# Kernel tuning notes

Measured on AMD Instinct MI355X. Metric: run time of the kernel, lower is better.

## Reference

```python
import jax, jax.numpy as jnp
import numpy as np

N_NODES = 50000
N_EDGES = 800000
NFEAT = 128
NHID = 64  # gc1: NFEAT -> 2*NHID, gc2: 2*NHID -> NHID


def setup_inputs() -> dict:
    key = jax.random.key(0)
    k1, k2, k3, k4, k5 = jax.random.split(key, 5)
    feat = jax.random.normal(k1, (N_NODES, NFEAT), dtype=jnp.float32)
    src = jax.random.randint(k2, (N_EDGES,), 0, N_NODES, dtype=jnp.int32)
    dst = jax.random.randint(k3, (N_EDGES,), 0, N_NODES, dtype=jnp.int32)
    # GraphConv weights: (in_feats, out_feats), xavier-like scale
    W1 = jax.random.normal(k4, (NFEAT, 2 * NHID), dtype=jnp.float32) / np.sqrt(NFEAT)
    b1 = jnp.zeros((2 * NHID,), dtype=jnp.float32)
    W2 = jax.random.normal(k5, (2 * NHID, NHID), dtype=jnp.float32) / np.sqrt(2 * NHID)
    b2 = jnp.zeros((NHID,), dtype=jnp.float32)
    return {"feat": feat, "src": src, "dst": dst, "W1": W1, "b1": b1, "W2": W2, "b2": b2}


def _graph_conv(feat, src, dst, W, b):
    """DGL GraphConv, norm='both', allow_zero_in_degree=True.
    h = D_in^{-1/2} A (D_out^{-1/2} x) W + b, with degrees clamped to >= 1.
    Applies W before aggregation when in_feats > out_feats (saves bandwidth)."""
    N = feat.shape[0]
    ones = jnp.ones(src.shape[0], dtype=feat.dtype)
    deg_out = jnp.clip(jax.ops.segment_sum(ones, src, num_segments=N), 1.0)
    deg_in = jnp.clip(jax.ops.segment_sum(ones, dst, num_segments=N), 1.0)
    h = feat * (deg_out ** -0.5)[:, None]
    mult_first = W.shape[0] > W.shape[1]
    if mult_first:
        h = h @ W
    agg = jax.ops.segment_sum(h[src], dst, num_segments=N)  # [N, d]
    if not mult_first:
        agg = agg @ W
    return agg * (deg_in ** -0.5)[:, None] + b


def reference(feat, src, dst, W1, b1, W2, b2):
    x = jax.nn.relu(_graph_conv(feat, src, dst, W1, b1))
    # dropout is inactive in eval mode (F.dropout training=False)
    x = _graph_conv(x, src, dst, W2, b2)
    return jax.nn.log_softmax(x, axis=1)
```

## Files before the change

### kernel.cpp

```cpp
#include <hip/hip_runtime.h>
#include <math.h>


constexpr int NF   = 128;
constexpr int NH   = 64;
constexpr int CAP  = 48;
constexpr int EPB  = 4096;
constexpr int BCAP = 8192;
constexpr int NBKMAX = 256;

typedef unsigned int uint;
typedef unsigned short ushort_t;
typedef __attribute__((ext_vector_type(8))) short short8;
typedef __attribute__((ext_vector_type(4))) float f32x4;

__device__ __forceinline__ float bflo(uint u) { return __uint_as_float(u << 16); }
__device__ __forceinline__ float bfhi(uint u) { return __uint_as_float(u & 0xffff0000u); }
__device__ __forceinline__ uint packbf(float a, float b) {
    uint ua = __float_as_uint(a), ub = __float_as_uint(b);
    uint ra = (ua + 0x7fffu + ((ua >> 16) & 1u)) >> 16;
    uint rb = (ub + 0x7fffu + ((ub >> 16) & 1u)) >> 16;
    return ra | (rb << 16);
}
__device__ __forceinline__ ushort_t bf16u(float f) {
    uint u = __float_as_uint(f);
    return (ushort_t)((u + 0x7fffu + ((u >> 16) & 1u)) >> 16);
}
__device__ __forceinline__ short8 as_short8(uint4 u) {
    union { uint4 u; short8 s; } x; x.u = u; return x.s;
}

__global__ __launch_bounds__(1024) void partition_kernel(
        const int* __restrict__ src, const int* __restrict__ dst,
        uint* __restrict__ pairs_g, ushort_t* __restrict__ srcb_g,
        int* __restrict__ dcur, int* __restrict__ scur,
        const float* __restrict__ W1, const float* __restrict__ W2,
        uint* __restrict__ W1p, uint* __restrict__ W2p,
        int E, int nbk, int nchunk) {
    if (blockIdx.x >= nchunk) {
        int i = (blockIdx.x - nchunk) * 1024 + threadIdx.x;
        if (i < 8192) {
            int jp = i & 3, g = (i >> 2) & 3, n = (i >> 4) & 127, kk = i >> 11;
            int k = kk * 32 + g * 8 + jp * 2;
            W1p[i] = packbf(W1[k * 128 + n], W1[(k + 1) * 128 + n]);
        } else if (i < 12288) {
            int j = i - 8192;
            int jp = j & 3, g = (j >> 2) & 3, n = (j >> 4) & 63, kk = j >> 10;
            int k = kk * 32 + g * 8 + jp * 2;
            W2p[j] = packbf(W2[k * 64 + n], W2[(k + 1) * 64 + n]);
        }
        return;
    }
    __shared__ uint     pl[EPB];
    __shared__ ushort_t sl[EPB];
    __shared__ int dh[NBKMAX], sh[NBKMAX];
    __shared__ int doff[NBKMAX], soff[NBKMAX];
    __shared__ int dbase[NBKMAX], sbase[NBKMAX];
    __shared__ int dpos[NBKMAX], spos[NBKMAX];
    int tid = threadIdx.x;
    int e0 = blockIdx.x * EPB;
    int ecnt = min(EPB, E - e0);

    for (int b = tid; b < nbk; b += 1024) { dh[b] = 0; sh[b] = 0; }
    __syncthreads();
    for (int i = tid; i < ecnt; i += 1024) {
        atomicAdd(&dh[dst[e0 + i] >> 8], 1);
        atomicAdd(&sh[src[e0 + i] >> 8], 1);
    }
    __syncthreads();
    if (tid < 128) {
        int wv = tid >> 6, l = tid & 63, b0 = l * 4;
        const int* h = wv ? sh : dh;
        int* of      = wv ? soff : doff;
        int v0 = (b0     < nbk) ? h[b0]     : 0;
        int v1 = (b0 + 1 < nbk) ? h[b0 + 1] : 0;
        int v2 = (b0 + 2 < nbk) ? h[b0 + 2] : 0;
        int v3 = (b0 + 3 < nbk) ? h[b0 + 3] : 0;
        int lsum = v0 + v1 + v2 + v3;
        int sc = lsum;
        #pragma unroll
        for (int off = 1; off < 64; off <<= 1) {
            int t = __shfl_up(sc, off, 64);
            if (l >= off) sc += t;
        }
        int excl = sc - lsum;
        if (b0     < nbk) of[b0]     = excl;
        if (b0 + 1 < nbk) of[b0 + 1] = excl + v0;
        if (b0 + 2 < nbk) of[b0 + 2] = excl + v0 + v1;
        if (b0 + 3 < nbk) of[b0 + 3] = excl + v0 + v1 + v2;
    }
    for (int b = tid; b < nbk; b += 1024) {
        dbase[b] = atomicAdd(&dcur[b], dh[b]);
        sbase[b] = atomicAdd(&scur[b], sh[b]);
    }
    __syncthreads();
    for (int b = tid; b < nbk; b += 1024) { dpos[b] = doff[b]; spos[b] = soff[b]; }
    __syncthreads();
    for (int i = tid; i < ecnt; i += 1024) {
        int s = src[e0 + i], d = dst[e0 + i];
        int p = atomicAdd(&dpos[d >> 8], 1);
        pl[p] = ((uint)s << 16) | (uint)d;
        int q = atomicAdd(&spos[s >> 8], 1);
        sl[q] = (ushort_t)s;
    }
    __syncthreads();
    for (int i = tid; i < ecnt; i += 1024) {
        uint e = pl[i];
        int b = (int)((e & 0xffffu) >> 8);
        int gp = dbase[b] + (i - doff[b]);
        if (gp < BCAP) pairs_g[(size_t)b * BCAP + gp] = e;
        ushort_t sv = sl[i];
        int b2 = (int)(sv >> 8);
        int gq = sbase[b2] + (i - soff[b2]);
        if (gq < BCAP) srcb_g[(size_t)b2 * BCAP + gq] = sv;
    }
}

__global__ __launch_bounds__(1024) void bin_kernel(
        const uint* __restrict__ pairs_g, const ushort_t* __restrict__ srcb_g,
        const int* __restrict__ dcur, const int* __restrict__ scur,
        const float* __restrict__ feat, uint* __restrict__ featb,
        ushort_t* __restrict__ slots, int* __restrict__ lens,
        float* __restrict__ s_in, float* __restrict__ s_out, int N) {
    __shared__ ushort_t slots_l[256 * CAP];
    __shared__ int cin[256], cout[256];
    __shared__ float souts[256];
    int tid = threadIdx.x;
    int b = blockIdx.x;
    int lo = b << 8;
    for (int r = tid; r < 256; r += 1024) { cin[r] = 0; cout[r] = 0; }
    __syncthreads();
    int dn = min(dcur[b], BCAP);
    for (int i = tid; i < dn; i += 1024) {
        uint e = pairs_g[(size_t)b * BCAP + i];
        int r = (int)(e & 255u);
        int p = atomicAdd(&cin[r], 1);
        if (p < CAP) slots_l[r * CAP + p] = (ushort_t)(e >> 16);
    }
    int sn = min(scur[b], BCAP);
    for (int i = tid; i < sn; i += 1024)
        atomicAdd(&cout[(int)srcb_g[(size_t)b * BCAP + i] - lo], 1);
    __syncthreads();
    int nrow = min(256, N - lo);
    {
        const uint4* sl4 = (const uint4*)slots_l;
        uint4* gs4 = (uint4*)(slots + (size_t)lo * CAP);
        int lim4 = nrow * (CAP / 8);
        for (int k = tid; k < 256 * CAP / 8; k += 1024)
            if (k < lim4) gs4[k] = sl4[k];
    }
    for (int r = tid; r < nrow; r += 1024) {
        int node = lo + r;
        int ci = cin[r];
        lens[node]  = min(ci, CAP);
        s_in[node]  = rsqrtf((float)max(ci, 1));
        float so    = rsqrtf((float)max(cout[r], 1));
        s_out[node] = so;
        souts[r]    = so;
    }
    __syncthreads();
    for (int k = tid; k < nrow * 16; k += 1024) {
        int r = k >> 4, ch = k & 15;
        float sc = souts[r];
        const float4* f4 = (const float4*)(feat + (size_t)(lo + r) * NF + ch * 8);
        float4 a = f4[0], c = f4[1];
        uint4 o;
        o.x = packbf(a.x * sc, a.y * sc);
        o.y = packbf(a.z * sc, a.w * sc);
        o.z = packbf(c.x * sc, c.y * sc);
        o.w = packbf(c.z * sc, c.w * sc);
        *(uint4*)(featb + (size_t)(lo + r) * 64 + ch * 4) = o;
    }
}

__global__ __launch_bounds__(256) void agg1_kernel(const uint* __restrict__ featb,
        const int* __restrict__ lens, const ushort_t* __restrict__ slots,
        uint* __restrict__ agg1b, int N) {
    int wave = threadIdx.x >> 6;
    int lane = threadIdx.x & 63;
    int q   = lane >> 4;
    int sub = lane & 15;
    int node = blockIdx.x * 4 + wave;
    if (node >= N) return;
    int beg = node * CAP;
    int len = lens[node];
    float acc[8] = {0.f, 0.f, 0.f, 0.f, 0.f, 0.f, 0.f, 0.f};
    if (len > 0) {
        int li = min(lane, len - 1);
        int sidx = (int)slots[beg + li];
        int quads = (len + 3) >> 2;
        #pragma unroll 4
        for (int k = 0; k < quads; ++k) {
            int e = 4 * k + q;
            int s = __shfl(sidx, e, 64);
            if (e < len) {
                uint4 v = *(const uint4*)(featb + (size_t)s * 64 + sub * 4);
                acc[0] += bflo(v.x); acc[1] += bfhi(v.x);
                acc[2] += bflo(v.y); acc[3] += bfhi(v.y);
                acc[4] += bflo(v.z); acc[5] += bfhi(v.z);
                acc[6] += bflo(v.w); acc[7] += bfhi(v.w);
            }
        }
    }
    #pragma unroll
    for (int j = 0; j < 8; ++j) {
        acc[j] += __shfl_xor(acc[j], 32, 64);
        acc[j] += __shfl_xor(acc[j], 16, 64);
    }
    if (q == 0) {
        uint4 o;
        o.x = packbf(acc[0], acc[1]);
        o.y = packbf(acc[2], acc[3]);
        o.z = packbf(acc[4], acc[5]);
        o.w = packbf(acc[6], acc[7]);
        *(uint4*)(agg1b + (size_t)node * 64 + sub * 4) = o;
    }
}

__global__ __launch_bounds__(256) void fused_gemm_kernel(
        const uint* __restrict__ agg1b, const uint* __restrict__ W1p,
        const float* __restrict__ b1, const uint* __restrict__ W2p,
        const float* __restrict__ s_in, const float* __restrict__ s_out,
        uint* __restrict__ h2b, int N) {
    __shared__ ushort_t x1t[64][136];
    __shared__ float sin_l[64], sout_l[64];
    int t = threadIdx.x;
    int base = blockIdx.x * 64;
    int w    = t >> 6;
    int lane = t & 63;
    int c = lane & 15;
    int g = lane >> 4;

    if (t < 64)       sin_l[t]        = (base + t < N) ? s_in[base + t] : 0.f;
    else if (t < 128) sout_l[t - 64]  = (base + t - 64 < N) ? s_out[base + t - 64] : 0.f;
    __syncthreads();

    f32x4 zero = {0.f, 0.f, 0.f, 0.f};
    f32x4 c1[4][2];
    #pragma unroll
    for (int mt = 0; mt < 4; ++mt) { c1[mt][0] = zero; c1[mt][1] = zero; }
    #pragma unroll
    for (int kk = 0; kk < 4; ++kk) {
        short8 bf[2];
        #pragma unroll
        for (int ntl = 0; ntl < 2; ++ntl) {
            int n = (2 * w + ntl) * 16 + c;
            bf[ntl] = as_short8(*(const uint4*)(W1p + (size_t)kk * 2048 + n * 16 + g * 4));
        }
        #pragma unroll
        for (int mt = 0; mt < 4; ++mt) {
            int row = base + mt * 16 + c;
            short8 af = as_short8(*(const uint4*)(agg1b + (size_t)row * 64 + kk * 16 + g * 4));
            c1[mt][0] = __builtin_amdgcn_mfma_f32_16x16x32_bf16(af, bf[0], c1[mt][0], 0, 0, 0);
            c1[mt][1] = __builtin_amdgcn_mfma_f32_16x16x32_bf16(af, bf[1], c1[mt][1], 0, 0, 0);
        }
    }
    float bias0 = b1[(2 * w) * 16 + c];
    float bias1 = b1[(2 * w + 1) * 16 + c];
    #pragma unroll
    for (int mt = 0; mt < 4; ++mt) {
        #pragma unroll
        for (int r = 0; r < 4; ++r) {
            int rl = mt * 16 + g * 4 + r;
            float si = sin_l[rl], so = sout_l[rl];
            x1t[rl][(2 * w) * 16 + c]     = bf16u(fmaxf(fmaf(si, c1[mt][0][r], bias0), 0.f) * so);
            x1t[rl][(2 * w + 1) * 16 + c] = bf16u(fmaxf(fmaf(si, c1[mt][1][r], bias1), 0.f) * so);
        }
    }
    __syncthreads();

    f32x4 c2[4];
    #pragma unroll
    for (int mt = 0; mt < 4; ++mt) c2[mt] = zero;
    #pragma unroll
    for (int kk = 0; kk < 4; ++kk) {
        int n = w * 16 + c;
        short8 bf2 = as_short8(*(const uint4*)(W2p + (size_t)kk * 1024 + n * 16 + g * 4));
        #pragma unroll
        for (int mt = 0; mt < 4; ++mt) {
            short8 af = *(const short8*)&x1t[mt * 16 + c][kk * 32 + g * 8];
            c2[mt] = __builtin_amdgcn_mfma_f32_16x16x32_bf16(af, bf2, c2[mt], 0, 0, 0);
        }
    }
    __syncthreads();

    ushort_t* h2t = &x1t[0][0];
    #pragma unroll
    for (int mt = 0; mt < 4; ++mt) {
        #pragma unroll
        for (int r = 0; r < 4; ++r) {
            int rl = mt * 16 + g * 4 + r;
            h2t[rl * 72 + w * 16 + c] = bf16u(c2[mt][r]);
        }
    }
    __syncthreads();
    int row = t >> 2, ch = t & 3;
    if (base + row < N) {
        uint4 v0 = *(const uint4*)(h2t + row * 72 + ch * 16);
        uint4 v1 = *(const uint4*)(h2t + row * 72 + ch * 16 + 8);
        *(uint4*)(h2b + (size_t)(base + row) * 32 + ch * 8)     = v0;
        *(uint4*)(h2b + (size_t)(base + row) * 32 + ch * 8 + 4) = v1;
    }
}

__global__ __launch_bounds__(256) void agg2_softmax_kernel(const uint* __restrict__ h2b,
        const int* __restrict__ lens, const ushort_t* __restrict__ slots,
        const float* __restrict__ s_in, const float* __restrict__ b2,
        float* __restrict__ out, int N) {
    int wave = threadIdx.x >> 6;
    int lane = threadIdx.x & 63;
    int oct = lane >> 3;
    int sub = lane & 7;
    int node = blockIdx.x * 4 + wave;
    if (node >= N) return;
    int beg = node * CAP;
    int len = lens[node];
    float acc[8] = {0.f, 0.f, 0.f, 0.f, 0.f, 0.f, 0.f, 0.f};
    if (len > 0) {
        int li = min(lane, len - 1);
        int sidx = (int)slots[beg + li];
        int octs = (len + 7) >> 3;
        #pragma unroll 4
        for (int k = 0; k < octs; ++k) {
            int e = 8 * k + oct;
            int s = __shfl(sidx, e, 64);
            if (e < len) {
                uint4 v = *(const uint4*)(h2b + (size_t)s * 32 + sub * 4);
                acc[0] += bflo(v.x); acc[1] += bfhi(v.x);
                acc[2] += bflo(v.y); acc[3] += bfhi(v.y);
                acc[4] += bflo(v.z); acc[5] += bfhi(v.z);
                acc[6] += bflo(v.w); acc[7] += bfhi(v.w);
            }
        }
    }
    #pragma unroll
    for (int j = 0; j < 8; ++j) {
        acc[j] += __shfl_xor(acc[j], 32, 64);
        acc[j] += __shfl_xor(acc[j], 16, 64);
        acc[j] += __shfl_xor(acc[j], 8, 64);
    }
    float si = s_in[node];
    float4 bb0 = *(const float4*)(b2 + sub * 8);
    float4 bb1 = *(const float4*)(b2 + sub * 8 + 4);
    float v[8];
    v[0] = fmaf(acc[0], si, bb0.x); v[1] = fmaf(acc[1], si, bb0.y);
    v[2] = fmaf(acc[2], si, bb0.z); v[3] = fmaf(acc[3], si, bb0.w);
    v[4] = fmaf(acc[4], si, bb1.x); v[5] = fmaf(acc[5], si, bb1.y);
    v[6] = fmaf(acc[6], si, bb1.z); v[7] = fmaf(acc[7], si, bb1.w);

    float m = v[0];
    #pragma unroll
    for (int j = 1; j < 8; ++j) m = fmaxf(m, v[j]);
    m = fmaxf(m, __shfl_xor(m, 4, 64));
    m = fmaxf(m, __shfl_xor(m, 2, 64));
    m = fmaxf(m, __shfl_xor(m, 1, 64));
    float s8 = 0.f;
    #pragma unroll
    for (int j = 0; j < 8; ++j) s8 += expf(v[j] - m);
    s8 += __shfl_xor(s8, 4, 64);
    s8 += __shfl_xor(s8, 2, 64);
    s8 += __shfl_xor(s8, 1, 64);
    float ls = m + logf(s8);
    if (oct == 0) {
        float4 o0 = make_float4(v[0] - ls, v[1] - ls, v[2] - ls, v[3] - ls);
        float4 o1 = make_float4(v[4] - ls, v[5] - ls, v[6] - ls, v[7] - ls);
        *(float4*)(out + (size_t)node * NH + sub * 8)     = o0;
        *(float4*)(out + (size_t)node * NH + sub * 8 + 4) = o1;
    }
}

extern "C" void kernel_launch(void* const* d_in, const int* in_sizes, int n_in,
                              void* d_out, int out_size, void* d_ws, size_t ws_size,
                              hipStream_t stream) {
    const float* feat = (const float*)d_in[0];
    const int*   src  = (const int*)d_in[1];
    const int*   dst  = (const int*)d_in[2];
    const float* W1   = (const float*)d_in[3];
    const float* b1   = (const float*)d_in[4];
    const float* W2   = (const float*)d_in[5];
    const float* b2   = (const float*)d_in[6];
    float* out = (float*)d_out;

    int N = in_sizes[0] / NF;
    int E = in_sizes[1];
    int nbk = (N + 255) >> 8;
    int nchunk = (E + EPB - 1) / EPB;
    int Npad = (N + 63) & ~63;

    char* p = (char*)d_ws;
    auto alloc = [&](size_t bytes) -> char* {
        char* q = p;
        p += (bytes + 255) & ~(size_t)255;
        return q;
    };
    int*      dcur  = (int*)alloc((size_t)nbk * 4);
    int*      scur  = (int*)alloc((size_t)nbk * 4);
    uint*     pairs = (uint*)alloc((size_t)nbk * BCAP * 4);
    ushort_t* srcb  = (ushort_t*)alloc((size_t)nbk * BCAP * 2);
    ushort_t* slots = (ushort_t*)alloc((size_t)N * CAP * 2);
    int*      lens  = (int*)alloc((size_t)N * 4);
    float*    s_out = (float*)alloc((size_t)N * 4);
    float*    s_in  = (float*)alloc((size_t)N * 4);
    uint*     featb = (uint*)alloc((size_t)N * 64 * 4);
    uint*     agg1b = (uint*)alloc((size_t)Npad * 64 * 4);
    uint*     W1p   = (uint*)alloc(8192 * 4);
    uint*     W2p   = (uint*)alloc(4096 * 4);
    uint*     h2b   = (uint*)alloc((size_t)N * 32 * 4);

    size_t cur_span = (size_t)((char*)scur - (char*)dcur) + (size_t)nbk * 4;
    hipMemsetAsync(dcur, 0, cur_span, stream);

    partition_kernel<<<nchunk + 12, 1024, 0, stream>>>(
        src, dst, pairs, srcb, dcur, scur, W1, W2, W1p, W2p, E, nbk, nchunk);
    bin_kernel<<<nbk, 1024, 0, stream>>>(pairs, srcb, dcur, scur, feat, featb,
                                         slots, lens, s_in, s_out, N);
    agg1_kernel<<<(N + 3) / 4, 256, 0, stream>>>(featb, lens, slots, agg1b, N);
    fused_gemm_kernel<<<(N + 63) / 64, 256, 0, stream>>>(agg1b, W1p, b1, W2p, s_in, s_out, h2b, N);
    agg2_softmax_kernel<<<(N + 3) / 4, 256, 0, stream>>>(h2b, lens, slots, s_in, b2, out, N);
}
```

Baseline: 176.9 us.

## Move feature bf16 cast into partition kernel and apply out-degree scale during gather

The fp32-to-bf16 conversion of node features moves from bin_kernel into 64 extra blocks of partition_kernel, so it no longer waits for the degree counts and can overlap with edge partitioning. Because the cast now happens before out-degree scaling is known, agg1 multiplies each gathered neighbor row by its s_out value with an FMA. This shortens bin_kernel's critical path, but agg1 now performs one extra scattered 4-byte load per edge, and rounding to bf16 happens before scaling rather than after.

```diff
diff --git a/kernel.cpp b/kernel.cpp
--- a/kernel.cpp
+++ b/kernel.cpp
@@ -8,6 +8,7 @@
 constexpr int EPB  = 4096;
 constexpr int BCAP = 8192;
 constexpr int NBKMAX = 256;
+constexpr int CASTB = 64;
 
 typedef unsigned int uint;
 typedef unsigned short ushort_t;
@@ -36,18 +37,35 @@
         int* __restrict__ dcur, int* __restrict__ scur,
         const float* __restrict__ W1, const float* __restrict__ W2,
         uint* __restrict__ W1p, uint* __restrict__ W2p,
-        int E, int nbk, int nchunk) {
+        const float* __restrict__ feat, uint* __restrict__ featb,
+        int E, int nbk, int nchunk, int N) {
     if (blockIdx.x >= nchunk) {
-        int i = (blockIdx.x - nchunk) * 1024 + threadIdx.x;
-        if (i < 8192) {
-            int jp = i & 3, g = (i >> 2) & 3, n = (i >> 4) & 127, kk = i >> 11;
-            int k = kk * 32 + g * 8 + jp * 2;
-            W1p[i] = packbf(W1[k * 128 + n], W1[(k + 1) * 128 + n]);
-        } else if (i < 12288) {
-            int j = i - 8192;
-            int jp = j & 3, g = (j >> 2) & 3, n = (j >> 4) & 63, kk = j >> 10;
-            int k = kk * 32 + g * 8 + jp * 2;
-            W2p[j] = packbf(W2[k * 64 + n], W2[(k + 1) * 64 + n]);
+        int xb = blockIdx.x - nchunk;
+        if (xb < 12) {
+            int i = xb * 1024 + threadIdx.x;
+            if (i < 8192) {
+                int jp = i & 3, g = (i >> 2) & 3, n = (i >> 4) & 127, kk = i >> 11;
+                int k = kk * 32 + g * 8 + jp * 2;
+                W1p[i] = packbf(W1[k * 128 + n], W1[(k + 1) * 128 + n]);
+            } else if (i < 12288) {
+                int j = i - 8192;
+                int jp = j & 3, g = (j >> 2) & 3, n = (j >> 4) & 63, kk = j >> 10;
+                int k = kk * 32 + g * 8 + jp * 2;
+                W2p[j] = packbf(W2[k * 64 + n], W2[(k + 1) * 64 + n]);
+            }
+        } else {
+            int items = N * 16;
+            for (int k = (xb - 12) * 1024 + threadIdx.x; k < items; k += CASTB * 1024) {
+                int r = k >> 4, ch = k & 15;
+                const float4* f4 = (const float4*)(feat + (size_t)r * NF + ch * 8);
+                float4 a = f4[0], c = f4[1];
+                uint4 o;
+                o.x = packbf(a.x, a.y);
+                o.y = packbf(a.z, a.w);
+                o.z = packbf(c.x, c.y);
+                o.w = packbf(c.z, c.w);
+                *(uint4*)(featb + (size_t)r * 64 + ch * 4) = o;
+            }
         }
         return;
     }
@@ -119,12 +137,10 @@
 __global__ __launch_bounds__(1024) void bin_kernel(
         const uint* __restrict__ pairs_g, const ushort_t* __restrict__ srcb_g,
         const int* __restrict__ dcur, const int* __restrict__ scur,
-        const float* __restrict__ feat, uint* __restrict__ featb,
         ushort_t* __restrict__ slots, int* __restrict__ lens,
         float* __restrict__ s_in, float* __restrict__ s_out, int N) {
     __shared__ ushort_t slots_l[256 * CAP];
     __shared__ int cin[256], cout[256];
-    __shared__ float souts[256];
     int tid = threadIdx.x;
     int b = blockIdx.x;
     int lo = b << 8;
@@ -154,28 +170,13 @@
         int ci = cin[r];
         lens[node]  = min(ci, CAP);
         s_in[node]  = rsqrtf((float)max(ci, 1));
-        float so    = rsqrtf((float)max(cout[r], 1));
-        s_out[node] = so;
-        souts[r]    = so;
-    }
-    __syncthreads();
-    for (int k = tid; k < nrow * 16; k += 1024) {
-        int r = k >> 4, ch = k & 15;
-        float sc = souts[r];
-        const float4* f4 = (const float4*)(feat + (size_t)(lo + r) * NF + ch * 8);
-        float4 a = f4[0], c = f4[1];
-        uint4 o;
-        o.x = packbf(a.x * sc, a.y * sc);
-        o.y = packbf(a.z * sc, a.w * sc);
-        o.z = packbf(c.x * sc, c.y * sc);
-        o.w = packbf(c.z * sc, c.w * sc);
-        *(uint4*)(featb + (size_t)(lo + r) * 64 + ch * 4) = o;
+        s_out[node] = rsqrtf((float)max(cout[r], 1));
     }
 }
 
 __global__ __launch_bounds__(256) void agg1_kernel(const uint* __restrict__ featb,
         const int* __restrict__ lens, const ushort_t* __restrict__ slots,
-        uint* __restrict__ agg1b, int N) {
+        const float* __restrict__ s_out, uint* __restrict__ agg1b, int N) {
     int wave = threadIdx.x >> 6;
     int lane = threadIdx.x & 63;
     int q   = lane >> 4;
@@ -194,11 +195,16 @@
             int e = 4 * k + q;
             int s = __shfl(sidx, e, 64);
             if (e < len) {
+                float so = s_out[s];
                 uint4 v = *(const uint4*)(featb + (size_t)s * 64 + sub * 4);
-                acc[0] += bflo(v.x); acc[1] += bfhi(v.x);
-                acc[2] += bflo(v.y); acc[3] += bfhi(v.y);
-                acc[4] += bflo(v.z); acc[5] += bfhi(v.z);
-                acc[6] += bflo(v.w); acc[7] += bfhi(v.w);
+                acc[0] = fmaf(so, bflo(v.x), acc[0]);
+                acc[1] = fmaf(so, bfhi(v.x), acc[1]);
+                acc[2] = fmaf(so, bflo(v.y), acc[2]);
+                acc[3] = fmaf(so, bfhi(v.y), acc[3]);
+                acc[4] = fmaf(so, bflo(v.z), acc[4]);
+                acc[5] = fmaf(so, bfhi(v.z), acc[5]);
+                acc[6] = fmaf(so, bflo(v.w), acc[6]);
+                acc[7] = fmaf(so, bfhi(v.w), acc[7]);
             }
         }
     }
@@ -410,11 +416,12 @@
     size_t cur_span = (size_t)((char*)scur - (char*)dcur) + (size_t)nbk * 4;
     hipMemsetAsync(dcur, 0, cur_span, stream);
 
-    partition_kernel<<<nchunk + 12, 1024, 0, stream>>>(
-        src, dst, pairs, srcb, dcur, scur, W1, W2, W1p, W2p, E, nbk, nchunk);
-    bin_kernel<<<nbk, 1024, 0, stream>>>(pairs, srcb, dcur, scur, feat, featb,
+    partition_kernel<<<nchunk + 12 + CASTB, 1024, 0, stream>>>(
+        src, dst, pairs, srcb, dcur, scur, W1, W2, W1p, W2p, feat, featb,
+        E, nbk, nchunk, N);
+    bin_kernel<<<nbk, 1024, 0, stream>>>(pairs, srcb, dcur, scur,
                                          slots, lens, s_in, s_out, N);
-    agg1_kernel<<<(N + 3) / 4, 256, 0, stream>>>(featb, lens, slots, agg1b, N);
+    agg1_kernel<<<(N + 3) / 4, 256, 0, stream>>>(featb, lens, slots, s_out, agg1b, N);
     fused_gemm_kernel<<<(N + 63) / 64, 256, 0, stream>>>(agg1b, W1p, b1, W2p, s_in, s_out, h2b, N);
     agg2_softmax_kernel<<<(N + 3) / 4, 256, 0, stream>>>(h2b, lens, slots, s_in, b2, out, N);
 }
```

Result: faster. 171.7 us (-2.9%).
